# Optimization experiments

Hardware: AMD Instinct MI355X
Metric: run time of the kernel (lower is better)

## Reference

```python
import jax, jax.numpy as jnp
import numpy as np

B, T, N, F_IN, F_OUT, K = 16, 12, 1024, 32, 64, 3


def _make_cheb(key, n, k):
    # random symmetric 'scaled laplacian' in [-1, 1]-ish, then Chebyshev recurrence
    a = jax.random.normal(key, (n, n), dtype=jnp.float32) * 0.02
    L = (a + a.T) * 0.5
    polys = [jnp.eye(n, dtype=jnp.float32), L]
    for i in range(2, k):
        polys.append(2.0 * L @ polys[-1] - polys[-2])
    return jnp.stack(polys[:k], axis=0)  # [K, N, N]


def setup_inputs() -> dict:
    key = jax.random.key(0)
    k1, k2, k3, k4 = jax.random.split(key, 4)
    x = jax.random.normal(k1, (B, T, N, F_IN), dtype=jnp.float32)
    spatial_attention = jax.random.uniform(k2, (B, N, N), dtype=jnp.float32)
    cheb = _make_cheb(k3, N, K)
    # xavier-uniform-ish init for Theta [K, F_in, F_out]
    limit = float(np.sqrt(6.0 / (F_IN + F_OUT)))
    Theta = jax.random.uniform(k4, (K, F_IN, F_OUT), dtype=jnp.float32,
                               minval=-limit, maxval=limit)
    return {"x": x, "spatial_attention": spatial_attention, "cheb": cheb, "Theta": Theta}


def reference(x, spatial_attention, cheb, Theta):
    # T_k_at[b,k,i,j] = cheb[k,i,j] * att[b,i,j]   (mask-multiply)
    tk_at = cheb[None, :, :, :] * spatial_attention[:, None, :, :]  # [B,K,N,N]
    # rhs[b,t,k,i,f] = sum_j tk_at[b,k,i,j] * x[b,t,j,f]
    rhs = jnp.einsum('bkij,btjf->btkif', tk_at, x)
    # out[b,t,i,o] = sum_{k,f} rhs[b,t,k,i,f] * Theta[k,f,o], then ReLU
    out = jnp.einsum('btkif,kfo->btio', rhs, Theta)
    return jax.nn.relu(out)
```

## Files before the change

kernel.cpp:

```cpp
#include <hip/hip_runtime.h>

#define Bb 16
#define Tt 12
#define Nn 1024
#define FIN 32
#define FOUT 64
#define KC 3
#define KJ (KC * Nn)
#define TF (Tt * FIN)
#define NO (Tt * FOUT)

#define BM 128
#define BN 192
#define BK 64
#define NKT (Nn / BK)

typedef __attribute__((ext_vector_type(8))) short short8;
typedef __attribute__((ext_vector_type(4))) float f32x4;

__device__ __forceinline__ unsigned short f2bf(float f) {
  union { float f; unsigned u; } v; v.f = f;
  unsigned r = v.u + 0x7FFFu + ((v.u >> 16) & 1u);
  return (unsigned short)(r >> 16);
}

__device__ __forceinline__ void BAR() {
  __builtin_amdgcn_sched_barrier(0);
  __builtin_amdgcn_s_barrier();
  __builtin_amdgcn_sched_barrier(0);
}

__global__ __launch_bounds__(256) void k1_build_A(
    const float* __restrict__ att, const float* __restrict__ cheb,
    unsigned short* __restrict__ Acat) {
  const unsigned idx = blockIdx.x * 256u + threadIdx.x;
  const int j = (idx & 127u) << 3;
  const int i = (idx >> 7) & 1023u;
  const int b = idx >> 17;
  const float* ap = att + ((size_t)b * Nn + i) * Nn + j;
  const float4 a0 = *(const float4*)ap;
  const float4 a1 = *(const float4*)(ap + 4);
  const size_t obase = ((size_t)b * Nn + i) * KJ + j;
#pragma unroll
  for (int k = 0; k < KC; ++k) {
    const float* cp = cheb + ((size_t)k * Nn + i) * Nn + j;
    const float4 c0 = *(const float4*)cp;
    const float4 c1 = *(const float4*)(cp + 4);
    short8 o;
    o[0] = (short)f2bf(a0.x * c0.x); o[1] = (short)f2bf(a0.y * c0.y);
    o[2] = (short)f2bf(a0.z * c0.z); o[3] = (short)f2bf(a0.w * c0.w);
    o[4] = (short)f2bf(a1.x * c1.x); o[5] = (short)f2bf(a1.y * c1.y);
    o[6] = (short)f2bf(a1.z * c1.z); o[7] = (short)f2bf(a1.w * c1.w);
    *(short8*)(Acat + obase + (size_t)k * Nn) = o;
  }
}

__global__ __launch_bounds__(256) void k2r_build_YxT(
    const float* __restrict__ x, unsigned short* __restrict__ YxT) {
  __shared__ float xs[256][33];
  const int tid = threadIdx.x;
  const int bid = blockIdx.x;
  const int jc = bid & 3;
  const int bt = bid >> 2;
  const int t = bt % Tt, b = bt / Tt;
  const int j0 = jc * 256;
  const float* xp = x + ((size_t)(b * Tt + t) * Nn + j0) * FIN;
#pragma unroll
  for (int m = 0; m < 8; ++m) {
    const int flat = m * 256 + tid;
    const int j_loc = flat >> 3, f4 = flat & 7;
    const float4 v = *(const float4*)(xp + (size_t)j_loc * FIN + f4 * 4);
    xs[j_loc][f4 * 4 + 0] = v.x; xs[j_loc][f4 * 4 + 1] = v.y;
    xs[j_loc][f4 * 4 + 2] = v.z; xs[j_loc][f4 * 4 + 3] = v.w;
  }
  __syncthreads();
  const int f = tid >> 3, jg = tid & 7;
  unsigned short* dst = YxT + ((size_t)b * TF + t * FIN + f) * Nn + j0 + jg * 32;
#pragma unroll
  for (int m = 0; m < 4; ++m) {
    short8 sh;
#pragma unroll
    for (int e = 0; e < 8; ++e)
      sh[e] = (short)f2bf(xs[jg * 32 + m * 8 + e][f]);
    *(short8*)(dst + m * 8) = sh;
  }
}

__global__ __launch_bounds__(512, 2) void k3r_gemm(
    const unsigned short* __restrict__ A, const unsigned short* __restrict__ YxT,
    unsigned short* __restrict__ rhs) {
  __shared__ __align__(16) unsigned short lds[40960];
  const int bid = blockIdx.x;
  const int logical = (bid & 7) * 96 + (bid >> 3);
  const int bk = logical >> 4;
  const int r  = logical & 15;
  const int it = r >> 1;
  const int nt = r & 1;
  const int b  = bk / 3, kk = bk % 3;
  const unsigned short* Ap = A + ((size_t)b * Nn + it * BM) * KJ + (size_t)kk * Nn;
  const unsigned short* Bp = YxT + ((size_t)b * TF + nt * BN) * Nn;
  const int tid = threadIdx.x;
  const int w = tid >> 6, l = tid & 63;
  const int wm = w >> 2, wn = w & 3;
  const int lrow = l & 15;
  const int c0 = l >> 4;
  const int sx = lrow & 7;

  f32x4 acc[4][3];
#pragma unroll
  for (int mi = 0; mi < 4; ++mi)
#pragma unroll
    for (int ni = 0; ni < 3; ++ni)
      acc[mi][ni] = (f32x4){0.f, 0.f, 0.f, 0.f};

  auto STAGE = [&](int d, int kt) {
    const int flat = w * 64 + l;
#pragma unroll
    for (int g = 0; g < 2; ++g) {
      const int idx = g * 512 + flat;
      const int row = idx >> 3;
      const int csrc = (idx & 7) ^ (row & 7);
      __builtin_amdgcn_global_load_lds(
          (const __attribute__((address_space(1))) void*)(Ap + (size_t)row * KJ + kt * BK + csrc * 8),
          (__attribute__((address_space(3))) void*)(lds + d * 8192 + (g * 512 + w * 64) * 8),
          16, 0, 0);
    }
#pragma unroll
    for (int g = 0; g < 3; ++g) {
      const int idx = g * 512 + flat;
      const int row = idx >> 3;
      const int csrc = (idx & 7) ^ (row & 7);
      __builtin_amdgcn_global_load_lds(
          (const __attribute__((address_space(1))) void*)(Bp + (size_t)row * Nn + kt * BK + csrc * 8),
          (__attribute__((address_space(3))) void*)(lds + 16384 + d * 12288 + (g * 512 + w * 64) * 8),
          16, 0, 0);
    }
  };

  auto LDA = [&](int d, int mi, int ks) -> short8 {
    const int row = wm * 64 + mi * 16 + lrow;
    const int ch  = (c0 | (ks << 2)) ^ sx;
    return *(const short8*)&lds[d * 8192 + row * 64 + ch * 8];
  };
  auto LDB = [&](int d, int ni, int ks) -> short8 {
    const int row = wn * 48 + ni * 16 + lrow;
    const int ch  = (c0 | (ks << 2)) ^ sx;
    return *(const short8*)&lds[16384 + d * 12288 + row * 64 + ch * 8];
  };

  STAGE(0, 0);
  STAGE(1, 1);
  asm volatile("s_waitcnt vmcnt(5)" ::: "memory");
  BAR();

  for (int tau = 0; tau < NKT; ++tau) {
    const int d = tau & 1;
    const bool dostage = (tau + 2 < NKT);
    short8 a0[4], b0[3], a1[4], b1[3];
#pragma unroll
    for (int mi = 0; mi < 4; ++mi) a0[mi] = LDA(d, mi, 0);
#pragma unroll
    for (int ni = 0; ni < 3; ++ni) b0[ni] = LDB(d, ni, 0);
#pragma unroll
    for (int mi = 0; mi < 4; ++mi) a1[mi] = LDA(d, mi, 1);
#pragma unroll
    for (int ni = 0; ni < 3; ++ni) b1[ni] = LDB(d, ni, 1);
    __builtin_amdgcn_sched_barrier(0);
    __builtin_amdgcn_s_setprio(1);
#pragma unroll
    for (int mi = 0; mi < 4; ++mi)
#pragma unroll
      for (int ni = 0; ni < 3; ++ni)
        acc[mi][ni] = __builtin_amdgcn_mfma_f32_16x16x32_bf16(a0[mi], b0[ni], acc[mi][ni], 0, 0, 0);
    __builtin_amdgcn_s_setprio(0);
    asm volatile("s_waitcnt vmcnt(0) lgkmcnt(0)" ::: "memory");
    BAR();
    if (dostage) STAGE(d, tau + 2);
    __builtin_amdgcn_sched_barrier(0);
    __builtin_amdgcn_s_setprio(1);
#pragma unroll
    for (int mi = 0; mi < 4; ++mi)
#pragma unroll
      for (int ni = 0; ni < 3; ++ni)
        acc[mi][ni] = __builtin_amdgcn_mfma_f32_16x16x32_bf16(a1[mi], b1[ni], acc[mi][ni], 0, 0, 0);
    __builtin_amdgcn_s_setprio(0);
  }
  asm volatile("s_waitcnt vmcnt(0)" ::: "memory");

  unsigned short* Cw = rhs + ((size_t)bk * Nn + it * BM) * TF + nt * BN;
#pragma unroll
  for (int mi = 0; mi < 4; ++mi) {
#pragma unroll
    for (int ni = 0; ni < 3; ++ni) {
      const int col = wn * 48 + ni * 16 + lrow;
      const int row0 = wm * 64 + mi * 16 + c0 * 4;
      unsigned short* op = Cw + (size_t)row0 * TF + col;
      f32x4 v = acc[mi][ni];
#pragma unroll
      for (int q = 0; q < 4; ++q)
        op[(size_t)q * TF] = f2bf(v[q]);
    }
  }
}

__global__ __launch_bounds__(256) void k4_epilogue(
    const unsigned short* __restrict__ rhs, const float* __restrict__ theta,
    float* __restrict__ out) {
  __shared__ float th[KC * FIN * FOUT];
  const int tid = threadIdx.x;
  for (int s = tid; s < KC * FIN * FOUT; s += 256) th[s] = theta[s];
  __syncthreads();
  const int bid = blockIdx.x;
  const int ic = bid & 3;
  const int bt = bid >> 2;
  const int t = bt % Tt, b = bt / Tt;
  const int w = tid >> 6, l = tid & 63;
  const int lrow = l & 15;
  const int c0 = l >> 4;
  const int i0 = ic * 256 + w * 64;

  short8 bfrag[KC][4];
#pragma unroll
  for (int ks = 0; ks < KC; ++ks)
#pragma unroll
    for (int oi = 0; oi < 4; ++oi) {
      short8 bf;
#pragma unroll
      for (int rr = 0; rr < 8; ++rr)
        bf[rr] = (short)f2bf(th[(ks * FIN + c0 * 8 + rr) * FOUT + oi * 16 + lrow]);
      bfrag[ks][oi] = bf;
    }

  f32x4 acc[4][4];
#pragma unroll
  for (int mi = 0; mi < 4; ++mi)
#pragma unroll
    for (int oi = 0; oi < 4; ++oi)
      acc[mi][oi] = (f32x4){0.f, 0.f, 0.f, 0.f};

#pragma unroll
  for (int ks = 0; ks < KC; ++ks) {
#pragma unroll
    for (int mi = 0; mi < 4; ++mi) {
      const short8 af = *(const short8*)(
          rhs + ((size_t)(b * KC + ks) * Nn + i0 + mi * 16 + lrow) * TF + t * FIN + c0 * 8);
#pragma unroll
      for (int oi = 0; oi < 4; ++oi)
        acc[mi][oi] = __builtin_amdgcn_mfma_f32_16x16x32_bf16(af, bfrag[ks][oi], acc[mi][oi], 0, 0, 0);
    }
  }

#pragma unroll
  for (int mi = 0; mi < 4; ++mi) {
#pragma unroll
    for (int oi = 0; oi < 4; ++oi) {
      const int row = i0 + mi * 16 + c0 * 4;
      float* op = out + ((size_t)(b * Tt + t) * Nn + row) * FOUT + oi * 16 + lrow;
      f32x4 v = acc[mi][oi];
#pragma unroll
      for (int q = 0; q < 4; ++q)
        op[(size_t)q * FOUT] = fmaxf(v[q], 0.f);
    }
  }
}

__global__ __launch_bounds__(128) void k_fallback(
    const float* __restrict__ x, const float* __restrict__ att,
    const float* __restrict__ cheb, const float* __restrict__ theta,
    float* __restrict__ out) {
  const int blk = blockIdx.x;
  const int i = blk & 1023;
  const int bt = blk >> 10;
  const int t = bt % Tt, b = bt / Tt;
  __shared__ float rhs[KC * FIN];
  const int tid = threadIdx.x;
  if (tid < KC * FIN) {
    const int k = tid >> 5, f = tid & 31;
    const float* ar = att + ((size_t)b * Nn + i) * Nn;
    const float* cr = cheb + ((size_t)k * Nn + i) * Nn;
    const float* xr = x + ((size_t)(b * Tt + t) * Nn) * FIN + f;
    float s = 0.f;
    for (int j = 0; j < Nn; ++j) s = fmaf(ar[j] * cr[j], xr[(size_t)j * FIN], s);
    rhs[tid] = s;
  }
  __syncthreads();
  if (tid < FOUT) {
    float a = 0.f;
#pragma unroll
    for (int kf = 0; kf < KC * FIN; ++kf) a = fmaf(rhs[kf], theta[kf * FOUT + tid], a);
    out[((size_t)(b * Tt + t) * Nn + i) * FOUT + tid] = fmaxf(a, 0.f);
  }
}

extern "C" void kernel_launch(void* const* d_in, const int* in_sizes, int n_in,
                              void* d_out, int out_size, void* d_ws, size_t ws_size,
                              hipStream_t stream) {
  const float* x     = (const float*)d_in[0];
  const float* att   = (const float*)d_in[1];
  const float* cheb  = (const float*)d_in[2];
  const float* theta = (const float*)d_in[3];
  float* out = (float*)d_out;

  const size_t needA  = (size_t)Bb * Nn * KJ * sizeof(unsigned short);
  const size_t needYx = (size_t)Bb * TF * Nn * sizeof(unsigned short);
  const size_t needR  = (size_t)Bb * KC * Nn * TF * sizeof(unsigned short);
  if (ws_size >= needA + needYx + needR) {
    unsigned short* Acat = (unsigned short*)d_ws;
    unsigned short* YxT  = (unsigned short*)((char*)d_ws + needA);
    unsigned short* rhs  = (unsigned short*)((char*)d_ws + needA + needYx);
    hipLaunchKernelGGL(k1_build_A, dim3(Bb * Nn * (Nn / 8) / 256), dim3(256), 0, stream,
                       att, cheb, Acat);
    hipLaunchKernelGGL(k2r_build_YxT, dim3(Bb * Tt * 4), dim3(256), 0, stream,
                       x, YxT);
    hipLaunchKernelGGL(k3r_gemm, dim3(48 * (Nn / BM) * (TF / BN)), dim3(512), 0, stream,
                       Acat, YxT, rhs);
    hipLaunchKernelGGL(k4_epilogue, dim3(Bb * Tt * 4), dim3(256), 0, stream,
                       rhs, theta, out);
  } else {
    hipLaunchKernelGGL(k_fallback, dim3(Bb * Tt * Nn), dim3(128), 0, stream,
                       x, att, cheb, theta, out);
  }
}
```

Before: 115.5 us.

## Fuse attention-Chebyshev product into GEMM A-tile staging via register prefetch

```diff
diff --git a/kernel.cpp b/kernel.cpp
--- a/kernel.cpp
+++ b/kernel.cpp
@@ -6,7 +6,6 @@
 #define FIN 32
 #define FOUT 64
 #define KC 3
-#define KJ (KC * Nn)
 #define TF (Tt * FIN)
 #define NO (Tt * FOUT)
 
@@ -28,31 +27,6 @@
   __builtin_amdgcn_sched_barrier(0);
   __builtin_amdgcn_s_barrier();
   __builtin_amdgcn_sched_barrier(0);
-}
-
-__global__ __launch_bounds__(256) void k1_build_A(
-    const float* __restrict__ att, const float* __restrict__ cheb,
-    unsigned short* __restrict__ Acat) {
-  const unsigned idx = blockIdx.x * 256u + threadIdx.x;
-  const int j = (idx & 127u) << 3;
-  const int i = (idx >> 7) & 1023u;
-  const int b = idx >> 17;
-  const float* ap = att + ((size_t)b * Nn + i) * Nn + j;
-  const float4 a0 = *(const float4*)ap;
-  const float4 a1 = *(const float4*)(ap + 4);
-  const size_t obase = ((size_t)b * Nn + i) * KJ + j;
-#pragma unroll
-  for (int k = 0; k < KC; ++k) {
-    const float* cp = cheb + ((size_t)k * Nn + i) * Nn + j;
-    const float4 c0 = *(const float4*)cp;
-    const float4 c1 = *(const float4*)(cp + 4);
-    short8 o;
-    o[0] = (short)f2bf(a0.x * c0.x); o[1] = (short)f2bf(a0.y * c0.y);
-    o[2] = (short)f2bf(a0.z * c0.z); o[3] = (short)f2bf(a0.w * c0.w);
-    o[4] = (short)f2bf(a1.x * c1.x); o[5] = (short)f2bf(a1.y * c1.y);
-    o[6] = (short)f2bf(a1.z * c1.z); o[7] = (short)f2bf(a1.w * c1.w);
-    *(short8*)(Acat + obase + (size_t)k * Nn) = o;
-  }
 }
 
 __global__ __launch_bounds__(256) void k2r_build_YxT(
@@ -86,9 +60,9 @@
   }
 }
 
-__global__ __launch_bounds__(512, 2) void k3r_gemm(
-    const unsigned short* __restrict__ A, const unsigned short* __restrict__ YxT,
-    unsigned short* __restrict__ rhs) {
+__global__ __launch_bounds__(512, 4) void k3f_gemm(
+    const float* __restrict__ att, const float* __restrict__ cheb,
+    const unsigned short* __restrict__ YxT, unsigned short* __restrict__ rhs) {
   __shared__ __align__(16) unsigned short lds[40960];
   const int bid = blockIdx.x;
   const int logical = (bid & 7) * 96 + (bid >> 3);
@@ -97,7 +71,8 @@
   const int it = r >> 1;
   const int nt = r & 1;
   const int b  = bk / 3, kk = bk % 3;
-  const unsigned short* Ap = A + ((size_t)b * Nn + it * BM) * KJ + (size_t)kk * Nn;
+  const float* Aa = att  + ((size_t)b  * Nn + it * BM) * Nn;
+  const float* Ac = cheb + ((size_t)kk * Nn + it * BM) * Nn;
   const unsigned short* Bp = YxT + ((size_t)b * TF + nt * BN) * Nn;
   const int tid = threadIdx.x;
   const int w = tid >> 6, l = tid & 63;
@@ -113,21 +88,44 @@
     for (int ni = 0; ni < 3; ++ni)
       acc[mi][ni] = (f32x4){0.f, 0.f, 0.f, 0.f};
 
-  auto STAGE = [&](int d, int kt) {
-    const int flat = w * 64 + l;
-#pragma unroll
-    for (int g = 0; g < 2; ++g) {
-      const int idx = g * 512 + flat;
-      const int row = idx >> 3;
-      const int csrc = (idx & 7) ^ (row & 7);
-      __builtin_amdgcn_global_load_lds(
-          (const __attribute__((address_space(1))) void*)(Ap + (size_t)row * KJ + kt * BK + csrc * 8),
-          (__attribute__((address_space(3))) void*)(lds + d * 8192 + (g * 512 + w * 64) * 8),
-          16, 0, 0);
-    }
+  float4 ra[4], rc[4];
+
+  auto ISSUE = [&](int kt) {
+#pragma unroll
+    for (int u = 0; u < 2; ++u) {
+      const int idx = u * 512 + tid;
+      const int row = idx >> 3, c = idx & 7;
+      const float* ap = Aa + (size_t)row * Nn + kt * BK + c * 8;
+      const float* cp = Ac + (size_t)row * Nn + kt * BK + c * 8;
+      ra[2 * u]     = *(const float4*)ap;
+      ra[2 * u + 1] = *(const float4*)(ap + 4);
+      rc[2 * u]     = *(const float4*)cp;
+      rc[2 * u + 1] = *(const float4*)(cp + 4);
+    }
+  };
+
+  auto CVTW = [&](int d) {
+#pragma unroll
+    for (int u = 0; u < 2; ++u) {
+      const int idx = u * 512 + tid;
+      const int row = idx >> 3, c = idx & 7;
+      short8 o;
+      o[0] = (short)f2bf(ra[2 * u].x * rc[2 * u].x);
+      o[1] = (short)f2bf(ra[2 * u].y * rc[2 * u].y);
+      o[2] = (short)f2bf(ra[2 * u].z * rc[2 * u].z);
+      o[3] = (short)f2bf(ra[2 * u].w * rc[2 * u].w);
+      o[4] = (short)f2bf(ra[2 * u + 1].x * rc[2 * u + 1].x);
+      o[5] = (short)f2bf(ra[2 * u + 1].y * rc[2 * u + 1].y);
+      o[6] = (short)f2bf(ra[2 * u + 1].z * rc[2 * u + 1].z);
+      o[7] = (short)f2bf(ra[2 * u + 1].w * rc[2 * u + 1].w);
+      *(short8*)&lds[d * 8192 + row * 64 + (c ^ (row & 7)) * 8] = o;
+    }
+  };
+
+  auto BDMA = [&](int d, int kt) {
 #pragma unroll
     for (int g = 0; g < 3; ++g) {
-      const int idx = g * 512 + flat;
+      const int idx = g * 512 + tid;
       const int row = idx >> 3;
       const int csrc = (idx & 7) ^ (row & 7);
       __builtin_amdgcn_global_load_lds(
@@ -148,42 +146,46 @@
     return *(const short8*)&lds[16384 + d * 12288 + row * 64 + ch * 8];
   };
 
-  STAGE(0, 0);
-  STAGE(1, 1);
-  asm volatile("s_waitcnt vmcnt(5)" ::: "memory");
+  ISSUE(0);
+  asm volatile("s_waitcnt vmcnt(0)" ::: "memory");
+  CVTW(0);
+  ISSUE(1);
+  BDMA(0, 0);
+  BDMA(1, 1);
+  asm volatile("s_waitcnt vmcnt(6)" ::: "memory");
+  CVTW(1);
+  ISSUE(2);
+  asm volatile("s_waitcnt vmcnt(0) lgkmcnt(0)" ::: "memory");
   BAR();
 
   for (int tau = 0; tau < NKT; ++tau) {
     const int d = tau & 1;
-    const bool dostage = (tau + 2 < NKT);
-    short8 a0[4], b0[3], a1[4], b1[3];
-#pragma unroll
-    for (int mi = 0; mi < 4; ++mi) a0[mi] = LDA(d, mi, 0);
-#pragma unroll
-    for (int ni = 0; ni < 3; ++ni) b0[ni] = LDB(d, ni, 0);
-#pragma unroll
-    for (int mi = 0; mi < 4; ++mi) a1[mi] = LDA(d, mi, 1);
-#pragma unroll
-    for (int ni = 0; ni < 3; ++ni) b1[ni] = LDB(d, ni, 1);
-    __builtin_amdgcn_sched_barrier(0);
+    short8 bf[3];
     __builtin_amdgcn_s_setprio(1);
 #pragma unroll
-    for (int mi = 0; mi < 4; ++mi)
+    for (int ni = 0; ni < 3; ++ni) bf[ni] = LDB(d, ni, 0);
+#pragma unroll
+    for (int mi = 0; mi < 4; ++mi) {
+      const short8 af = LDA(d, mi, 0);
 #pragma unroll
       for (int ni = 0; ni < 3; ++ni)
-        acc[mi][ni] = __builtin_amdgcn_mfma_f32_16x16x32_bf16(a0[mi], b0[ni], acc[mi][ni], 0, 0, 0);
+        acc[mi][ni] = __builtin_amdgcn_mfma_f32_16x16x32_bf16(af, bf[ni], acc[mi][ni], 0, 0, 0);
+    }
+#pragma unroll
+    for (int ni = 0; ni < 3; ++ni) bf[ni] = LDB(d, ni, 1);
+#pragma unroll
+    for (int mi = 0; mi < 4; ++mi) {
+      const short8 af = LDA(d, mi, 1);
+#pragma unroll
+      for (int ni = 0; ni < 3; ++ni)
+        acc[mi][ni] = __builtin_amdgcn_mfma_f32_16x16x32_bf16(af, bf[ni], acc[mi][ni], 0, 0, 0);
+    }
     __builtin_amdgcn_s_setprio(0);
     asm volatile("s_waitcnt vmcnt(0) lgkmcnt(0)" ::: "memory");
     BAR();
-    if (dostage) STAGE(d, tau + 2);
+    if (tau + 2 < NKT) { CVTW(d); BDMA(d, tau + 2); }
+    if (tau + 3 < NKT) ISSUE(tau + 3);
     __builtin_amdgcn_sched_barrier(0);
-    __builtin_amdgcn_s_setprio(1);
-#pragma unroll
-    for (int mi = 0; mi < 4; ++mi)
-#pragma unroll
-      for (int ni = 0; ni < 3; ++ni)
-        acc[mi][ni] = __builtin_amdgcn_mfma_f32_16x16x32_bf16(a1[mi], b1[ni], acc[mi][ni], 0, 0, 0);
-    __builtin_amdgcn_s_setprio(0);
   }
   asm volatile("s_waitcnt vmcnt(0)" ::: "memory");
 
@@ -301,19 +303,15 @@
   const float* theta = (const float*)d_in[3];
   float* out = (float*)d_out;
 
-  const size_t needA  = (size_t)Bb * Nn * KJ * sizeof(unsigned short);
   const size_t needYx = (size_t)Bb * TF * Nn * sizeof(unsigned short);
   const size_t needR  = (size_t)Bb * KC * Nn * TF * sizeof(unsigned short);
-  if (ws_size >= needA + needYx + needR) {
-    unsigned short* Acat = (unsigned short*)d_ws;
-    unsigned short* YxT  = (unsigned short*)((char*)d_ws + needA);
-    unsigned short* rhs  = (unsigned short*)((char*)d_ws + needA + needYx);
-    hipLaunchKernelGGL(k1_build_A, dim3(Bb * Nn * (Nn / 8) / 256), dim3(256), 0, stream,
-                       att, cheb, Acat);
+  if (ws_size >= needYx + needR) {
+    unsigned short* YxT = (unsigned short*)d_ws;
+    unsigned short* rhs = (unsigned short*)((char*)d_ws + needYx);
     hipLaunchKernelGGL(k2r_build_YxT, dim3(Bb * Tt * 4), dim3(256), 0, stream,
                        x, YxT);
-    hipLaunchKernelGGL(k3r_gemm, dim3(48 * (Nn / BM) * (TF / BN)), dim3(512), 0, stream,
-                       Acat, YxT, rhs);
+    hipLaunchKernelGGL(k3f_gemm, dim3(48 * (Nn / BM) * (TF / BN)), dim3(512), 0, stream,
+                       att, cheb, YxT, rhs);
     hipLaunchKernelGGL(k4_epilogue, dim3(Bb * Tt * 4), dim3(256), 0, stream,
                        rhs, theta, out);
   } else {
```

After: 106.9 us. 1.08x faster.
